# Optimization experiments

Hardware: AMD Instinct MI355X
Metric: run time of the kernel (lower is better)

Reference implementation:

```python
import jax, jax.numpy as jnp
import numpy as np

N_NODES = 20000
N_EDGES = 640000
IN_F = 128
CL1_F = 128
CL2_F = 128
OUT_F = 2


def setup_inputs() -> dict:
    key = jax.random.key(0)
    ks = jax.random.split(key, 8)
    x = jax.random.normal(ks[0], (N_NODES, IN_F), dtype=jnp.float32)
    edge_index = jax.random.randint(ks[1], (2, N_EDGES), 0, N_NODES, dtype=jnp.int64)
    s1 = 1.0 / np.sqrt(IN_F)
    s2 = 1.0 / np.sqrt(CL1_F)
    s3 = 1.0 / np.sqrt(CL2_F)
    W1 = jax.random.uniform(ks[2], (IN_F, CL1_F), jnp.float32, -s1, s1)
    b1 = jax.random.uniform(ks[3], (CL1_F,), jnp.float32, -s1, s1)
    W2 = jax.random.uniform(ks[4], (CL1_F, CL2_F), jnp.float32, -s2, s2)
    b2 = jax.random.uniform(ks[5], (CL2_F,), jnp.float32, -s2, s2)
    W3 = jax.random.uniform(ks[6], (CL2_F, OUT_F), jnp.float32, -s3, s3)
    b3 = jax.random.uniform(ks[7], (OUT_F,), jnp.float32, -s3, s3)
    return {"x": x, "edge_index": edge_index, "W1": W1, "b1": b1,
            "W2": W2, "b2": b2, "W3": W3, "b3": b3}


def _scatter_mean(feat_src, src, dst, n_nodes):
    # out[i] = mean over edges e with dst[e]==i of feat_src gathered at src[e]
    msg = feat_src[src]                                   # [E, F] gather
    summed = jax.ops.segment_sum(msg, dst, num_segments=n_nodes)  # [N, F]
    ones = jnp.ones((src.shape[0],), dtype=feat_src.dtype)
    cnt = jax.ops.segment_sum(ones, dst, num_segments=n_nodes)    # [N]
    return summed / jnp.maximum(cnt, 1.0)[:, None]


def _mpnn_layer(x, src, dst, W, b, n_nodes):
    aggr = _scatter_mean(x, src, dst, n_nodes)
    return jax.nn.relu(aggr @ W + b)


def reference(x, edge_index, W1, b1, W2, b2, W3, b3):
    src, dst = edge_index[0], edge_index[1]
    n = x.shape[0]
    h = _mpnn_layer(x, src, dst, W1, b1, n)   # conv1 (update relu); extra relu is no-op
    h = _mpnn_layer(h, src, dst, W2, b2, n)   # conv2
    # dropout in eval mode is identity
    return h @ W3 + b3
```

## Files before the change

kernel.cpp:

```cpp
#include <hip/hip_runtime.h>

#define N_NODES 20000
#define N_EDGES 640000
#define F 128
#define CAP 128


__global__ __launch_bounds__(256)
void bucket_kernel(const int* __restrict__ src, const int* __restrict__ dst,
                   int* __restrict__ cnt, int* __restrict__ bucket) {
    int e = blockIdx.x * blockDim.x + threadIdx.x;
    if (e >= N_EDGES) return;
    int d = dst[e];
    int pos = atomicAdd(&cnt[d], 1);
    if (pos < CAP) bucket[(size_t)d * CAP + pos] = src[e];
}

__global__ __launch_bounds__(256)
void agg_mean_kernel(const float* __restrict__ feat, const int* __restrict__ cnt,
                     const int* __restrict__ bucket, float* __restrict__ out) {
    int wid  = (blockIdx.x * blockDim.x + threadIdx.x) >> 6;
    int lane = threadIdx.x & 63;
    if (wid >= N_NODES) return;
    int deg = cnt[wid];
    const int* lst = bucket + (size_t)wid * CAP;
    const float2* f2 = (const float2*)feat;
    float ax = 0.f, ay = 0.f;
    int j = 0;
    for (; j + 8 <= deg; j += 8) {
        int4 i0 = *(const int4*)(lst + j);
        int4 i1 = *(const int4*)(lst + j + 4);
        float2 v0 = f2[(size_t)i0.x * 64 + lane];
        float2 v1 = f2[(size_t)i0.y * 64 + lane];
        float2 v2 = f2[(size_t)i0.z * 64 + lane];
        float2 v3 = f2[(size_t)i0.w * 64 + lane];
        float2 v4 = f2[(size_t)i1.x * 64 + lane];
        float2 v5 = f2[(size_t)i1.y * 64 + lane];
        float2 v6 = f2[(size_t)i1.z * 64 + lane];
        float2 v7 = f2[(size_t)i1.w * 64 + lane];
        ax += (v0.x + v1.x) + (v2.x + v3.x) + ((v4.x + v5.x) + (v6.x + v7.x));
        ay += (v0.y + v1.y) + (v2.y + v3.y) + ((v4.y + v5.y) + (v6.y + v7.y));
    }
    for (; j < deg; ++j) {
        float2 v = f2[(size_t)lst[j] * 64 + lane];
        ax += v.x; ay += v.y;
    }
    float sc = 1.0f / fmaxf((float)deg, 1.0f);
    float2 o; o.x = ax * sc; o.y = ay * sc;
    ((float2*)out)[(size_t)wid * 64 + lane] = o;
}

__global__ __launch_bounds__(256)
void gemm_bias_relu_kernel(const float* __restrict__ A, const float* __restrict__ W,
                           const float* __restrict__ b, float* __restrict__ C) {
    __shared__ float As[32][F + 4];
    int tid  = threadIdx.x;
    int row0 = blockIdx.x * 32;

    const float4* A4 = (const float4*)(A + (size_t)row0 * F);
    for (int i = tid; i < 32 * 32; i += 256) {
        float4 v = A4[i];
        int r = i >> 5, c4 = (i & 31) * 4;
        *(float4*)&As[r][c4] = v;
    }
    __syncthreads();

    int tx = tid & 31, ty = tid >> 5;
    int c0 = tx * 4, r0 = ty * 4;
    float acc[4][4] = {};

    for (int k = 0; k < F; k += 4) {
        float4 a4[4];
#pragma unroll
        for (int i = 0; i < 4; ++i) a4[i] = *(const float4*)&As[r0 + i][k];
#pragma unroll
        for (int u = 0; u < 4; ++u) {
            float4 w = *(const float4*)(W + (size_t)(k + u) * F + c0);
#pragma unroll
            for (int i = 0; i < 4; ++i) {
                float a = (u == 0) ? a4[i].x : (u == 1) ? a4[i].y : (u == 2) ? a4[i].z : a4[i].w;
                acc[i][0] += a * w.x;
                acc[i][1] += a * w.y;
                acc[i][2] += a * w.z;
                acc[i][3] += a * w.w;
            }
        }
    }

    float4 bias = *(const float4*)(b + c0);
#pragma unroll
    for (int i = 0; i < 4; ++i) {
        float4 o;
        o.x = fmaxf(acc[i][0] + bias.x, 0.f);
        o.y = fmaxf(acc[i][1] + bias.y, 0.f);
        o.z = fmaxf(acc[i][2] + bias.z, 0.f);
        o.w = fmaxf(acc[i][3] + bias.w, 0.f);
        *(float4*)(C + (size_t)(row0 + r0 + i) * F + c0) = o;
    }
}

__global__ __launch_bounds__(256)
void final_kernel(const float* __restrict__ h, const float* __restrict__ W3,
                  const float* __restrict__ b3, float* __restrict__ out) {
    int wid  = (blockIdx.x * blockDim.x + threadIdx.x) >> 6;
    int lane = threadIdx.x & 63;
    if (wid >= N_NODES) return;
    float2 v = ((const float2*)h)[(size_t)wid * 64 + lane];
    float4 w = ((const float4*)W3)[lane];
    float a0 = v.x * w.x + v.y * w.z;
    float a1 = v.x * w.y + v.y * w.w;
#pragma unroll
    for (int off = 32; off > 0; off >>= 1) {
        a0 += __shfl_down(a0, off);
        a1 += __shfl_down(a1, off);
    }
    if (lane == 0) {
        out[(size_t)wid * 2]     = a0 + b3[0];
        out[(size_t)wid * 2 + 1] = a1 + b3[1];
    }
}

extern "C" void kernel_launch(void* const* d_in, const int* in_sizes, int n_in,
                              void* d_out, int out_size, void* d_ws, size_t ws_size,
                              hipStream_t stream) {
    const float* x   = (const float*)d_in[0];
    const int*   ei  = (const int*)d_in[1];
    const int*   src = ei;
    const int*   dst = ei + N_EDGES;
    const float* W1 = (const float*)d_in[2];
    const float* b1 = (const float*)d_in[3];
    const float* W2 = (const float*)d_in[4];
    const float* b2 = (const float*)d_in[5];
    const float* W3 = (const float*)d_in[6];
    const float* b3 = (const float*)d_in[7];
    float* out = (float*)d_out;

    char* base = (char*)d_ws;
    size_t off = 0;
    auto take = [&](size_t bytes) -> char* {
        char* p = base + off;
        off += (bytes + 255) & ~(size_t)255;
        return p;
    };
    int*   cnt    = (int*)  take(N_NODES * sizeof(int));
    int*   bucket = (int*)  take((size_t)N_NODES * CAP * sizeof(int));
    float* aggr   = (float*)take((size_t)N_NODES * F * sizeof(float));
    float* h      = (float*)take((size_t)N_NODES * F * sizeof(float));

    hipMemsetAsync(cnt, 0, N_NODES * sizeof(int), stream);
    bucket_kernel<<<(N_EDGES + 255) / 256, 256, 0, stream>>>(src, dst, cnt, bucket);

    agg_mean_kernel<<<(N_NODES * 64 + 255) / 256, 256, 0, stream>>>(x, cnt, bucket, aggr);
    gemm_bias_relu_kernel<<<N_NODES / 32, 256, 0, stream>>>(aggr, W1, b1, h);
    agg_mean_kernel<<<(N_NODES * 64 + 255) / 256, 256, 0, stream>>>(h, cnt, bucket, aggr);
    gemm_bias_relu_kernel<<<N_NODES / 32, 256, 0, stream>>>(aggr, W2, b2, aggr);
    final_kernel<<<(N_NODES * 64 + 255) / 256, 256, 0, stream>>>(aggr, W3, b3, out);
}
```

Before: 218.2 us.

## Fuse mean aggregation into GEMM layer kernel with half-wave float4 gathers

Merges the gather-mean aggregation and the bias+ReLU GEMM into one kernel per layer. Each block aggregates 32 nodes straight into shared memory before the matmul, so the aggregated features no longer make a round trip through global memory and two launches go away. The gather now splits each wave into two halves that each take alternate neighbors with float4 loads, then combines them with a shuffle. In exchange, each block loops serially over 8 nodes per wave, and the GEMM phase cannot start until the gather finishes, which may reduce latency hiding.

```diff
diff --git a/kernel.cpp b/kernel.cpp
--- a/kernel.cpp
+++ b/kernel.cpp
@@ -4,6 +4,7 @@
 #define N_EDGES 640000
 #define F 128
 #define CAP 128
+#define ROWS 32
 
 
 __global__ __launch_bounds__(256)
@@ -17,57 +18,77 @@
 }
 
 __global__ __launch_bounds__(256)
-void agg_mean_kernel(const float* __restrict__ feat, const int* __restrict__ cnt,
-                     const int* __restrict__ bucket, float* __restrict__ out) {
-    int wid  = (blockIdx.x * blockDim.x + threadIdx.x) >> 6;
-    int lane = threadIdx.x & 63;
-    if (wid >= N_NODES) return;
-    int deg = cnt[wid];
-    const int* lst = bucket + (size_t)wid * CAP;
-    const float2* f2 = (const float2*)feat;
-    float ax = 0.f, ay = 0.f;
-    int j = 0;
-    for (; j + 8 <= deg; j += 8) {
-        int4 i0 = *(const int4*)(lst + j);
-        int4 i1 = *(const int4*)(lst + j + 4);
-        float2 v0 = f2[(size_t)i0.x * 64 + lane];
-        float2 v1 = f2[(size_t)i0.y * 64 + lane];
-        float2 v2 = f2[(size_t)i0.z * 64 + lane];
-        float2 v3 = f2[(size_t)i0.w * 64 + lane];
-        float2 v4 = f2[(size_t)i1.x * 64 + lane];
-        float2 v5 = f2[(size_t)i1.y * 64 + lane];
-        float2 v6 = f2[(size_t)i1.z * 64 + lane];
-        float2 v7 = f2[(size_t)i1.w * 64 + lane];
-        ax += (v0.x + v1.x) + (v2.x + v3.x) + ((v4.x + v5.x) + (v6.x + v7.x));
-        ay += (v0.y + v1.y) + (v2.y + v3.y) + ((v4.y + v5.y) + (v6.y + v7.y));
-    }
-    for (; j < deg; ++j) {
-        float2 v = f2[(size_t)lst[j] * 64 + lane];
-        ax += v.x; ay += v.y;
-    }
-    float sc = 1.0f / fmaxf((float)deg, 1.0f);
-    float2 o; o.x = ax * sc; o.y = ay * sc;
-    ((float2*)out)[(size_t)wid * 64 + lane] = o;
-}
+void fused_layer_kernel(const float* __restrict__ feat, const int* __restrict__ cnt,
+                        const int* __restrict__ bucket, const float* __restrict__ W,
+                        const float* __restrict__ b, float* __restrict__ out) {
+    __shared__ float As[ROWS][F + 4];
+    int tid  = threadIdx.x;
+    int wave = tid >> 6;
+    int lane = tid & 63;
+    int half = lane >> 5;
+    int sub  = lane & 31;
+    int row0 = blockIdx.x * ROWS;
 
-__global__ __launch_bounds__(256)
-void gemm_bias_relu_kernel(const float* __restrict__ A, const float* __restrict__ W,
-                           const float* __restrict__ b, float* __restrict__ C) {
-    __shared__ float As[32][F + 4];
-    int tid  = threadIdx.x;
-    int row0 = blockIdx.x * 32;
+    const float4* f4 = (const float4*)feat;
 
-    const float4* A4 = (const float4*)(A + (size_t)row0 * F);
-    for (int i = tid; i < 32 * 32; i += 256) {
-        float4 v = A4[i];
-        int r = i >> 5, c4 = (i & 31) * 4;
-        *(float4*)&As[r][c4] = v;
+    for (int t = 0; t < 8; ++t) {
+        int nl   = wave * 8 + t;
+        int node = row0 + nl;
+        int deg  = cnt[node];
+        const int* lst = bucket + (size_t)node * CAP;
+        float4 acc; acc.x = acc.y = acc.z = acc.w = 0.f;
+        int j = 0;
+        for (; j + 16 <= deg; j += 16) {
+            int4 ia = *(const int4*)(lst + j);
+            int4 ib = *(const int4*)(lst + j + 4);
+            int4 ic = *(const int4*)(lst + j + 8);
+            int4 id = *(const int4*)(lst + j + 12);
+            int i0 = half ? ia.y : ia.x;
+            int i1 = half ? ia.w : ia.z;
+            int i2 = half ? ib.y : ib.x;
+            int i3 = half ? ib.w : ib.z;
+            int i4 = half ? ic.y : ic.x;
+            int i5 = half ? ic.w : ic.z;
+            int i6 = half ? id.y : id.x;
+            int i7 = half ? id.w : id.z;
+            float4 v0 = f4[(size_t)i0 * 32 + sub];
+            float4 v1 = f4[(size_t)i1 * 32 + sub];
+            float4 v2 = f4[(size_t)i2 * 32 + sub];
+            float4 v3 = f4[(size_t)i3 * 32 + sub];
+            float4 v4 = f4[(size_t)i4 * 32 + sub];
+            float4 v5 = f4[(size_t)i5 * 32 + sub];
+            float4 v6 = f4[(size_t)i6 * 32 + sub];
+            float4 v7 = f4[(size_t)i7 * 32 + sub];
+            acc.x += ((v0.x + v1.x) + (v2.x + v3.x)) + ((v4.x + v5.x) + (v6.x + v7.x));
+            acc.y += ((v0.y + v1.y) + (v2.y + v3.y)) + ((v4.y + v5.y) + (v6.y + v7.y));
+            acc.z += ((v0.z + v1.z) + (v2.z + v3.z)) + ((v4.z + v5.z) + (v6.z + v7.z));
+            acc.w += ((v0.w + v1.w) + (v2.w + v3.w)) + ((v4.w + v5.w) + (v6.w + v7.w));
+        }
+        for (; j + 2 <= deg; j += 2) {
+            int2 ii = *(const int2*)(lst + j);
+            int idx = half ? ii.y : ii.x;
+            float4 v = f4[(size_t)idx * 32 + sub];
+            acc.x += v.x; acc.y += v.y; acc.z += v.z; acc.w += v.w;
+        }
+        if (j < deg && half == 0) {
+            float4 v = f4[(size_t)lst[j] * 32 + sub];
+            acc.x += v.x; acc.y += v.y; acc.z += v.z; acc.w += v.w;
+        }
+        acc.x += __shfl(acc.x, lane ^ 32);
+        acc.y += __shfl(acc.y, lane ^ 32);
+        acc.z += __shfl(acc.z, lane ^ 32);
+        acc.w += __shfl(acc.w, lane ^ 32);
+        if (half == 0) {
+            float inv = 1.0f / fmaxf((float)deg, 1.0f);
+            float4 o; o.x = acc.x * inv; o.y = acc.y * inv; o.z = acc.z * inv; o.w = acc.w * inv;
+            *(float4*)&As[nl][sub * 4] = o;
+        }
     }
     __syncthreads();
 
     int tx = tid & 31, ty = tid >> 5;
     int c0 = tx * 4, r0 = ty * 4;
-    float acc[4][4] = {};
+    float acc2[4][4] = {};
 
     for (int k = 0; k < F; k += 4) {
         float4 a4[4];
@@ -79,10 +100,10 @@
 #pragma unroll
             for (int i = 0; i < 4; ++i) {
                 float a = (u == 0) ? a4[i].x : (u == 1) ? a4[i].y : (u == 2) ? a4[i].z : a4[i].w;
-                acc[i][0] += a * w.x;
-                acc[i][1] += a * w.y;
-                acc[i][2] += a * w.z;
-                acc[i][3] += a * w.w;
+                acc2[i][0] += a * w.x;
+                acc2[i][1] += a * w.y;
+                acc2[i][2] += a * w.z;
+                acc2[i][3] += a * w.w;
             }
         }
     }
@@ -91,11 +112,11 @@
 #pragma unroll
     for (int i = 0; i < 4; ++i) {
         float4 o;
-        o.x = fmaxf(acc[i][0] + bias.x, 0.f);
-        o.y = fmaxf(acc[i][1] + bias.y, 0.f);
-        o.z = fmaxf(acc[i][2] + bias.z, 0.f);
-        o.w = fmaxf(acc[i][3] + bias.w, 0.f);
-        *(float4*)(C + (size_t)(row0 + r0 + i) * F + c0) = o;
+        o.x = fmaxf(acc2[i][0] + bias.x, 0.f);
+        o.y = fmaxf(acc2[i][1] + bias.y, 0.f);
+        o.z = fmaxf(acc2[i][2] + bias.z, 0.f);
+        o.w = fmaxf(acc2[i][3] + bias.w, 0.f);
+        *(float4*)(out + (size_t)(row0 + r0 + i) * F + c0) = o;
     }
 }
 
@@ -144,15 +165,13 @@
     };
     int*   cnt    = (int*)  take(N_NODES * sizeof(int));
     int*   bucket = (int*)  take((size_t)N_NODES * CAP * sizeof(int));
-    float* aggr   = (float*)take((size_t)N_NODES * F * sizeof(float));
-    float* h      = (float*)take((size_t)N_NODES * F * sizeof(float));
+    float* h1     = (float*)take((size_t)N_NODES * F * sizeof(float));
+    float* h2     = (float*)take((size_t)N_NODES * F * sizeof(float));
 
     hipMemsetAsync(cnt, 0, N_NODES * sizeof(int), stream);
     bucket_kernel<<<(N_EDGES + 255) / 256, 256, 0, stream>>>(src, dst, cnt, bucket);
 
-    agg_mean_kernel<<<(N_NODES * 64 + 255) / 256, 256, 0, stream>>>(x, cnt, bucket, aggr);
-    gemm_bias_relu_kernel<<<N_NODES / 32, 256, 0, stream>>>(aggr, W1, b1, h);
-    agg_mean_kernel<<<(N_NODES * 64 + 255) / 256, 256, 0, stream>>>(h, cnt, bucket, aggr);
-    gemm_bias_relu_kernel<<<N_NODES / 32, 256, 0, stream>>>(aggr, W2, b2, aggr);
-    final_kernel<<<(N_NODES * 64 + 255) / 256, 256, 0, stream>>>(aggr, W3, b3, out);
+    fused_layer_kernel<<<N_NODES / ROWS, 256, 0, stream>>>(x, cnt, bucket, W1, b1, h1);
+    fused_layer_kernel<<<N_NODES / ROWS, 256, 0, stream>>>(h1, cnt, bucket, W2, b2, h2);
+    final_kernel<<<(N_NODES * 64 + 255) / 256, 256, 0, stream>>>(h2, W3, b3, out);
 }
```

New measurement: 227.0 us. 1.04x slower.
